# Kernel tuning notes

Hardware: AMD Instinct MI355X
Metric: run time of the kernel (lower is better)

## Reference

```python
import jax, jax.numpy as jnp
import numpy as np

N_NODES = 50000
N_EDGES = 800000
D_IN = 128
D_OUT = 128


def setup_inputs() -> dict:
    key = jax.random.key(0)
    k1, k2, k3, k4 = jax.random.split(key, 4)
    node_features = jax.random.normal(k1, (N_NODES, D_IN), dtype=jnp.float32)
    edge_index = jax.random.randint(k2, (2, N_EDGES), 0, N_NODES, dtype=jnp.int64)
    # nn.Linear params: weight [out, in], bias [out]
    W = jax.random.normal(k3, (D_OUT, D_IN), dtype=jnp.float32) / np.sqrt(D_IN)
    b = jax.random.normal(k4, (D_OUT,), dtype=jnp.float32) * 0.01
    return {"node_features": node_features, "edge_index": edge_index, "W": W, "b": b}


def reference(node_features, edge_index, W, b):
    source_nodes = edge_index[0]
    dest_nodes = edge_index[1]
    # gather neighbor features [E, D_in], scatter-add into [N, D_in]
    neighbor_features = node_features[source_nodes]
    aggregated = jax.ops.segment_sum(neighbor_features, dest_nodes,
                                     num_segments=node_features.shape[0])
    # nn.Linear: x @ W.T + b
    return aggregated @ W.T + b
```

## Files before the change

kernel.cpp:

```cpp
#include <hip/hip_runtime.h>


constexpr int NN = 50000;
constexpr int NE = 800000;
constexpr int D  = 128;

constexpr int BS   = 128;
constexpr int NB   = (NN + BS - 1) / BS;
constexpr int EPB  = 4096;
constexpr int NSB  = (NE + EPB - 1) / EPB;
constexpr int CAP  = 4096;

constexpr int AROWU = 136;

typedef __attribute__((ext_vector_type(8))) short bf16x8;
typedef __attribute__((ext_vector_type(4))) float f32x4;

__device__ inline unsigned short f2bf(float f) {
    unsigned u = __float_as_uint(f);
    return (unsigned short)((u + 0x7fffu + ((u >> 16) & 1u)) >> 16);
}
__device__ inline float bflo(unsigned v) { return __uint_as_float(v << 16); }
__device__ inline float bfhi(unsigned v) { return __uint_as_float(v & 0xffff0000u); }

constexpr int NF4 = NN * D / 4;
constexpr int W4  = D * D / 4;
constexpr int NBLK_P = (NF4 + W4 + 511) / 512;
constexpr int GRID_A = NSB + NBLK_P;

__global__ __launch_bounds__(512) void k_prep_bucket(
    const float* __restrict__ nf, const float* __restrict__ W,
    const int* __restrict__ ei,
    ushort* __restrict__ nfh, ushort* __restrict__ Wh,
    ushort* __restrict__ offs, unsigned* __restrict__ buf)
{
    __shared__ int hist[NB], off[NB], cur[NB];
    __shared__ unsigned spk[EPB];
    const int t = threadIdx.x;

    if (blockIdx.x < NSB) {
        const int blk = blockIdx.x;
        const int e0  = blk * EPB;
        int cnt = NE - e0; if (cnt > EPB) cnt = EPB;

        for (int i = t; i < NB; i += 512) hist[i] = 0;
        __syncthreads();

        unsigned pk[8];
        #pragma unroll
        for (int j = 0; j < 8; ++j) {
            int idx = j * 512 + t;
            if (idx < cnt) {
                int e = e0 + idx;
                unsigned s = (unsigned)ei[e];
                unsigned d = (unsigned)ei[NE + e];
                pk[j] = (d << 16) | s;
                atomicAdd(&hist[pk[j] >> 23], 1);
            }
        }
        __syncthreads();
        if (t < NB) off[t] = hist[t];
        __syncthreads();
        for (int o = 1; o < NB; o <<= 1) {
            int v = (t >= o && t < NB) ? off[t - o] : 0;
            __syncthreads();
            if (t < NB) off[t] += v;
            __syncthreads();
        }
        if (t < NB) {
            int ex = off[t] - hist[t];
            cur[t] = ex;
            offs[blk * (NB + 1) + t] = (ushort)ex;
        }
        if (t == 0) offs[blk * (NB + 1) + NB] = (ushort)cnt;
        __syncthreads();
        #pragma unroll
        for (int j = 0; j < 8; ++j) {
            int idx = j * 512 + t;
            if (idx < cnt) {
                int l = atomicAdd(&cur[pk[j] >> 23], 1);
                spk[l] = pk[j];
            }
        }
        __syncthreads();
        for (int i = t; i < cnt; i += 512)
            buf[(size_t)blk * EPB + i] = spk[i];
    } else {
        int i = (blockIdx.x - NSB) * 512 + t;
        if (i < NF4) {
            float4 v = ((const float4*)nf)[i];
            ((ushort4*)nfh)[i] = make_ushort4(f2bf(v.x), f2bf(v.y), f2bf(v.z), f2bf(v.w));
        } else if (i < NF4 + W4) {
            int k = i - NF4;
            float4 v = ((const float4*)W)[k];
            ((ushort4*)Wh)[k] = make_ushort4(f2bf(v.x), f2bf(v.y), f2bf(v.z), f2bf(v.w));
        }
    }
}

__global__ __launch_bounds__(1024) void k_sort_agg(
    const unsigned* __restrict__ nfh, const unsigned* __restrict__ buf,
    const ushort* __restrict__ offs, const ushort* __restrict__ Wh,
    const float* __restrict__ bias, float* __restrict__ out)
{
    __shared__ unsigned pkbuf[CAP];
    __shared__ ushort srt[CAP];
    __shared__ int scnt[256];
    __shared__ int sbase[NSB], rbase[NSB];
    __shared__ int hist[BS], off[BS], cur[BS];
    __shared__ unsigned tile[BS * AROWU / 2];
    const int b = blockIdx.x, t = threadIdx.x;
    const int lane = t & 63, w = t >> 6;

    int my = 0;
    if (t < NSB) {
        int o0 = (int)offs[t * (NB + 1) + b];
        int o1 = (int)offs[t * (NB + 1) + b + 1];
        rbase[t] = o0;
        my = o1 - o0;
    }
    if (t < 256) scnt[t] = (t < NSB) ? my : 0;
    if (t < BS) hist[t] = 0;
    __syncthreads();
    for (int o = 1; o < 256; o <<= 1) {
        int v = (t >= o && t < 256) ? scnt[t - o] : 0;
        __syncthreads();
        if (t < 256) scnt[t] += v;
        __syncthreads();
    }
    if (t < NSB) sbase[t] = scnt[t] - my;
    __syncthreads();
    int total = scnt[NSB - 1];
    if (total > CAP) total = CAP;

    for (int p = t; p < total; p += 1024) {
        int lo = 0, hi = NSB - 1;
        while (lo < hi) {
            int mid = (lo + hi) >> 1;
            if (scnt[mid] > p) hi = mid; else lo = mid + 1;
        }
        unsigned pk = buf[(size_t)lo * EPB + rbase[lo] + (p - sbase[lo])];
        pkbuf[p] = pk;
        atomicAdd(&hist[(pk >> 16) & (BS - 1)], 1);
    }
    __syncthreads();

    if (t < BS) off[t] = hist[t];
    __syncthreads();
    for (int o = 1; o < BS; o <<= 1) {
        int v = (t >= o && t < BS) ? off[t - o] : 0;
        __syncthreads();
        if (t < BS) off[t] += v;
        __syncthreads();
    }
    if (t < BS) { int ex = off[t] - hist[t]; off[t] = ex; cur[t] = ex; }
    __syncthreads();
    for (int e = t; e < total; e += 1024) {
        unsigned pk = pkbuf[e];
        int n = (pk >> 16) & (BS - 1);
        int p = atomicAdd(&cur[n], 1);
        srt[p] = (ushort)(pk & 0xffffu);
    }
    __syncthreads();

    #pragma unroll
    for (int i = 0; i < 8; ++i) {
        const int n = w * 8 + i;
        const int beg = off[n], e = beg + hist[n];
        float ax=0.f, ay=0.f, bx=0.f, by=0.f, cx=0.f, cy=0.f, dx=0.f, dy=0.f;
        for (int p = beg; p < e; p += 8) {
            const int lim = e - 1;
            unsigned v[8];
            #pragma unroll
            for (int j = 0; j < 8; ++j) {
                int pos = p + j;
                bool ok = pos <= lim;
                if (!ok) pos = lim;
                unsigned s = srt[pos];
                unsigned val = nfh[(size_t)s * 64 + lane];
                v[j] = ok ? val : 0u;
            }
            ax += bflo(v[0]); ay += bfhi(v[0]);
            bx += bflo(v[1]); by += bfhi(v[1]);
            cx += bflo(v[2]); cy += bfhi(v[2]);
            dx += bflo(v[3]); dy += bfhi(v[3]);
            ax += bflo(v[4]); ay += bfhi(v[4]);
            bx += bflo(v[5]); by += bfhi(v[5]);
            cx += bflo(v[6]); cy += bfhi(v[6]);
            dx += bflo(v[7]); dy += bfhi(v[7]);
        }
        float rx = (ax + bx) + (cx + dx);
        float ry = (ay + by) + (cy + dy);
        tile[n * (AROWU / 2) + lane] =
            (unsigned)f2bf(rx) | ((unsigned)f2bf(ry) << 16);
    }
    __syncthreads();

    const int m = lane & 15, q = lane >> 4;
    const ushort* lds = (const ushort*)tile;
    #pragma unroll
    for (int i = 0; i < 4; ++i) {
        const int task = w + 16 * i;
        const int t16  = task >> 3;
        const int c0   = (task & 7) * 16;
        const int grow0 = b * BS + t16 * 16;
        if (grow0 < NN) {
            bf16x8 a[4];
            const ushort* arow = lds + (t16 * 16 + m) * AROWU + q * 8;
            #pragma unroll
            for (int kk = 0; kk < 4; ++kk)
                a[kk] = *(const bf16x8*)(arow + kk * 32);
            float bv = bias[c0 + m];
            f32x4 acc = { bv, bv, bv, bv };
            const ushort* wrow = Wh + (size_t)(c0 + m) * D + q * 8;
            #pragma unroll
            for (int kk = 0; kk < 4; ++kk) {
                bf16x8 bb = *(const bf16x8*)(wrow + kk * 32);
                acc = __builtin_amdgcn_mfma_f32_16x16x32_bf16(a[kk], bb, acc, 0, 0, 0);
            }
            float* op = out + (size_t)(grow0 + q * 4) * D + c0 + m;
            op[0]     = acc[0];
            op[D]     = acc[1];
            op[2 * D] = acc[2];
            op[3 * D] = acc[3];
        }
    }
}

extern "C" void kernel_launch(void* const* d_in, const int* in_sizes, int n_in,
                              void* d_out, int out_size, void* d_ws, size_t ws_size,
                              hipStream_t stream) {
    const float* nf = (const float*)d_in[0];
    const int*   ei = (const int*)d_in[1];
    const float* W  = (const float*)d_in[2];
    const float* b  = (const float*)d_in[3];
    float* out = (float*)d_out;

    ushort*   nfh  = (ushort*)d_ws;
    ushort*   Wh   = nfh + (size_t)NN * D;
    unsigned* buf  = (unsigned*)(Wh + D * D);
    ushort*   offs = (ushort*)(buf + (size_t)NSB * EPB);

    k_prep_bucket<<<GRID_A, 512, 0, stream>>>(nf, W, ei, nfh, Wh, offs, buf);
    k_sort_agg   <<<NB, 1024, 0, stream>>>((const unsigned*)nfh, buf, offs, Wh, b, out);
}
```

Before: 136.4 us.

## Gather neighbor rows with 16-byte loads across four edges per wave

The aggregation loop now has each group of 16 lanes load a full 256-byte bf16 row with uint4 loads, so a wave processes four edges at once instead of one 4-byte word per lane per edge. Partial sums are combined across the four lane groups with xor shuffles before the packed row is written to shared memory. The intent is to issue fewer, wider global loads and keep more independent gathers in flight. It adds cross-lane shuffle work, more per-lane accumulators, an unroll-1 outer loop and a min-blocks hint in the launch bounds.

```diff
diff --git a/kernel.cpp b/kernel.cpp
--- a/kernel.cpp
+++ b/kernel.cpp
@@ -98,7 +98,7 @@
     }
 }
 
-__global__ __launch_bounds__(1024) void k_sort_agg(
+__global__ __launch_bounds__(1024, 8) void k_sort_agg(
     const unsigned* __restrict__ nfh, const unsigned* __restrict__ buf,
     const ushort* __restrict__ offs, const ushort* __restrict__ Wh,
     const float* __restrict__ bias, float* __restrict__ out)
@@ -108,7 +108,7 @@
     __shared__ int scnt[256];
     __shared__ int sbase[NSB], rbase[NSB];
     __shared__ int hist[BS], off[BS], cur[BS];
-    __shared__ unsigned tile[BS * AROWU / 2];
+    __shared__ __align__(16) unsigned tile[BS * AROWU / 2];
     const int b = blockIdx.x, t = threadIdx.x;
     const int lane = t & 63, w = t >> 6;
 
@@ -163,36 +163,56 @@
     }
     __syncthreads();
 
-    #pragma unroll
+    const int qq = lane >> 4;
+    const int sl = lane & 15;
+    const uint4* nfv = (const uint4*)nfh;
+
+    #pragma unroll 1
     for (int i = 0; i < 8; ++i) {
         const int n = w * 8 + i;
         const int beg = off[n], e = beg + hist[n];
-        float ax=0.f, ay=0.f, bx=0.f, by=0.f, cx=0.f, cy=0.f, dx=0.f, dy=0.f;
-        for (int p = beg; p < e; p += 8) {
+        float accA[8] = {0,0,0,0,0,0,0,0};
+        float accB[8] = {0,0,0,0,0,0,0,0};
+        for (int p = beg; p < e; p += 16) {
             const int lim = e - 1;
-            unsigned v[8];
-            #pragma unroll
-            for (int j = 0; j < 8; ++j) {
-                int pos = p + j;
+            uint4 v[4];
+            #pragma unroll
+            for (int j = 0; j < 4; ++j) {
+                int pos = p + 4 * j + qq;
                 bool ok = pos <= lim;
                 if (!ok) pos = lim;
-                unsigned s = srt[pos];
-                unsigned val = nfh[(size_t)s * 64 + lane];
-                v[j] = ok ? val : 0u;
-            }
-            ax += bflo(v[0]); ay += bfhi(v[0]);
-            bx += bflo(v[1]); by += bfhi(v[1]);
-            cx += bflo(v[2]); cy += bfhi(v[2]);
-            dx += bflo(v[3]); dy += bfhi(v[3]);
-            ax += bflo(v[4]); ay += bfhi(v[4]);
-            bx += bflo(v[5]); by += bfhi(v[5]);
-            cx += bflo(v[6]); cy += bfhi(v[6]);
-            dx += bflo(v[7]); dy += bfhi(v[7]);
-        }
-        float rx = (ax + bx) + (cx + dx);
-        float ry = (ay + by) + (cy + dy);
-        tile[n * (AROWU / 2) + lane] =
-            (unsigned)f2bf(rx) | ((unsigned)f2bf(ry) << 16);
+                int s = srt[pos];
+                uint4 val = nfv[(size_t)s * 16 + sl];
+                v[j].x = ok ? val.x : 0u;
+                v[j].y = ok ? val.y : 0u;
+                v[j].z = ok ? val.z : 0u;
+                v[j].w = ok ? val.w : 0u;
+            }
+            #pragma unroll
+            for (int j = 0; j < 4; ++j) {
+                float* A = (j & 1) ? accB : accA;
+                A[0] += bflo(v[j].x); A[1] += bfhi(v[j].x);
+                A[2] += bflo(v[j].y); A[3] += bfhi(v[j].y);
+                A[4] += bflo(v[j].z); A[5] += bfhi(v[j].z);
+                A[6] += bflo(v[j].w); A[7] += bfhi(v[j].w);
+            }
+        }
+        float r[8];
+        #pragma unroll
+        for (int k = 0; k < 8; ++k) {
+            float x = accA[k] + accB[k];
+            x += __shfl_xor(x, 16);
+            x += __shfl_xor(x, 32);
+            r[k] = x;
+        }
+        if (qq == 0) {
+            uint4 o;
+            o.x = (unsigned)f2bf(r[0]) | ((unsigned)f2bf(r[1]) << 16);
+            o.y = (unsigned)f2bf(r[2]) | ((unsigned)f2bf(r[3]) << 16);
+            o.z = (unsigned)f2bf(r[4]) | ((unsigned)f2bf(r[5]) << 16);
+            o.w = (unsigned)f2bf(r[6]) | ((unsigned)f2bf(r[7]) << 16);
+            *(uint4*)(tile + n * (AROWU / 2) + sl * 4) = o;
+        }
     }
     __syncthreads();
 
```

After: 134.0 us. About the same (-1.7%).
